# Kernel tuning notes

Measured on AMD Instinct MI355X. Metric: run time of the kernel, lower is better.

## Reference

```python
import jax, jax.numpy as jnp
import numpy as np

N = 20000   # nodes
E = 320000  # edges (before self-loops)
D = 128     # hidden_dim (= per-head out channels, concat=False)
H = 4       # heads
NEG_SLOPE = 0.2   # GATv2 leaky_relu default
LN_EPS = 1e-5


def setup_inputs() -> dict:
    key = jax.random.key(0)
    ks = jax.random.split(key, 12)
    s = 0.05
    w = lambda k, shp: (jax.random.normal(k, shp, jnp.float32) * s)
    return {
        "x": jax.random.normal(ks[0], (N, D), jnp.float32),
        "src": jax.random.randint(ks[1], (E,), 0, N, jnp.int32),
        "dst": jax.random.randint(ks[2], (E,), 0, N, jnp.int32),
        "Wl1": w(ks[3], (D, H * D)), "Wr1": w(ks[4], (D, H * D)),
        "att1": w(ks[5], (H, D)), "b1": jnp.zeros((D,), jnp.float32),
        "g1": jnp.ones((D,), jnp.float32), "be1": jnp.zeros((D,), jnp.float32),
        "Wl2": w(ks[6], (D, H * D)), "Wr2": w(ks[7], (D, H * D)),
        "att2": w(ks[8], (H, D)), "b2": jnp.zeros((D,), jnp.float32),
        "g2": jnp.ones((D,), jnp.float32), "be2": jnp.zeros((D,), jnp.float32),
    }


def gatv2_conv(x, src, dst, Wl, Wr, att, bias):
    """GATv2Conv with concat=False (mean over heads), share_weights=False."""
    n = x.shape[0]
    xl = (x @ Wl).reshape(n, H, D)  # source-side projection
    xr = (x @ Wr).reshape(n, H, D)  # target-side projection
    m = jax.nn.leaky_relu(xl[src] + xr[dst], NEG_SLOPE)     # [E', H, D]
    e = jnp.einsum('ehd,hd->eh', m, att)                     # [E', H]
    # segment softmax over edges grouped by destination node
    e_max = jax.ops.segment_max(e, dst, num_segments=n)      # [N, H]
    ex = jnp.exp(e - e_max[dst])
    denom = jax.ops.segment_sum(ex, dst, num_segments=n)     # [N, H]
    alpha = ex / (denom[dst] + 1e-16)                        # [E', H]
    out = jax.ops.segment_sum(alpha[:, :, None] * xl[src], dst, num_segments=n)
    return out.mean(axis=1) + bias                           # [N, D]


def layer_norm(x, g, b):
    mu = x.mean(axis=-1, keepdims=True)
    var = ((x - mu) ** 2).mean(axis=-1, keepdims=True)
    return (x - mu) * jax.lax.rsqrt(var + LN_EPS) * g + b


def reference(x, src, dst, Wl1, Wr1, att1, b1, g1, be1,
              Wl2, Wr2, att2, b2, g2, be2):
    n = x.shape[0]
    # PyG GATv2Conv default add_self_loops=True
    loops = jnp.arange(n, dtype=src.dtype)
    s = jnp.concatenate([src, loops])
    d = jnp.concatenate([dst, loops])

    h = gatv2_conv(x, s, d, Wl1, Wr1, att1, b1)
    h = layer_norm(h, g1, be1)
    h = jax.nn.relu(h + x)

    h2 = gatv2_conv(h, s, d, Wl2, Wr2, att2, b2)
    h2 = layer_norm(h2, g2, be2)
    return h2 + h
```

## Files before the change

kernel.cpp:

```cpp
#include <hip/hip_runtime.h>
#include <hip/hip_bf16.h>
#include <hip/hip_fp16.h>

#define NNODES 20000
#define MPAD   20480
#define NEDGES 320000
#define DIM    128
#define NH     4
#define ETOT   (NEDGES + NNODES)
#define LN_EPS 1e-5f

typedef unsigned char  u8;
typedef unsigned short u16;
typedef unsigned int   u32;

typedef _Float16 f16x2 __attribute__((ext_vector_type(2)));
typedef _Float16 f16x8 __attribute__((ext_vector_type(8)));
typedef float    f32x2 __attribute__((ext_vector_type(2)));
typedef float    f32x4 __attribute__((ext_vector_type(4)));

__device__ inline u16 f2h(float f) {
    _Float16 h = (_Float16)f;
    union { _Float16 h; u16 u; } v; v.h = h; return v.u;
}
__device__ inline f16x2 u2h2(u32 u) { union { u32 u; f16x2 h; } v; v.u = u; return v.h; }
__device__ inline u32 h22u(f16x2 h) { union { f16x2 h; u32 u; } v; v.h = h; return v.u; }
__device__ inline f16x2 habs2(f16x2 h) { return u2h2(h22u(h) & 0x7FFF7FFFu); }

#define GLDS16(g, l) __builtin_amdgcn_global_load_lds(                         \
    (const __attribute__((address_space(1))) void*)(g),                        \
    (__attribute__((address_space(3))) void*)(l), 16, 0, 0)


__global__ __launch_bounds__(256) void k_prep(const float* __restrict__ x, u16* __restrict__ xb,
                       const float* __restrict__ Wl1, const float* __restrict__ Wr1,
                       u16* __restrict__ Bt1,
                       const float* __restrict__ Wl2, const float* __restrict__ Wr2,
                       u16* __restrict__ Bt2,
                       int* __restrict__ deg) {
    const int b = blockIdx.x, t = threadIdx.x;
    const int gid = b * 256 + t;
    if (gid < NNODES) deg[gid] = 1;

    for (int j = gid; j < NNODES * 32; j += 256 * 256) {
        float4 v = ((const float4*)x)[j];
        ushort4 o;
        o.x = f2h(v.x); o.y = f2h(v.y); o.z = f2h(v.z); o.w = f2h(v.w);
        ((ushort4*)xb)[j] = o;
    }

    {
        const int m    = b >> 6;
        const int tile = b & 63;
        const int kt   = tile >> 4;
        const int nt   = tile & 15;
        const float* W = (m == 0) ? Wl1 : (m == 1) ? Wr1 : (m == 2) ? Wl2 : Wr2;
        u16* Bt        = (m < 2) ? Bt1 : Bt2;
        const int nbase = (m & 1) * 512 + nt * 32;

        __shared__ float lds[32][33];
        const int tx = t & 31, ty = t >> 5;
#pragma unroll
        for (int i = 0; i < 4; ++i) {
            int k = kt * 32 + ty + i * 8;
            lds[ty + i * 8][tx] = W[k * 512 + nt * 32 + tx];
        }
        __syncthreads();
#pragma unroll
        for (int i = 0; i < 4; ++i) {
            int nrow = nbase + ty + i * 8;
            Bt[nrow * 128 + kt * 32 + tx] = f2h(lds[tx][ty + i * 8]);
        }
    }
}


__global__ void k_hist(const int* __restrict__ dst, int* __restrict__ deg) {
    int i = blockIdx.x * blockDim.x + threadIdx.x;
    if (i < NEDGES) atomicAdd(&deg[dst[i]], 1);
}

__global__ __launch_bounds__(1024) void k_scan(const int* __restrict__ deg,
                                               int* __restrict__ row,
                                               int* __restrict__ cur) {
    __shared__ int part[1024];
    const int CH = 20;
    int t = threadIdx.x;
    int base = t * CH;
    int s = 0;
    int d[20];
    if (base < NNODES) {
#pragma unroll
        for (int q = 0; q < 5; ++q) {
            int4 v = ((const int4*)(deg + base))[q];
            d[q*4+0] = v.x; d[q*4+1] = v.y; d[q*4+2] = v.z; d[q*4+3] = v.w;
            s += v.x + v.y + v.z + v.w;
        }
    }
    part[t] = s;
    __syncthreads();
    for (int off = 1; off < 1024; off <<= 1) {
        int v = (t >= off) ? part[t - off] : 0;
        __syncthreads();
        part[t] += v;
        __syncthreads();
    }
    if (base < NNODES) {
        int run = (t == 0) ? 0 : part[t - 1];
#pragma unroll
        for (int i = 0; i < CH; i++) {
            row[base + i] = run; cur[base + i] = run; run += d[i];
        }
    }
    if (t == 1023) row[NNODES] = part[1023];
}

__global__ void k_scatter(const int* __restrict__ src, const int* __restrict__ dst,
                          int* __restrict__ col, int* __restrict__ cur) {
    int i = blockIdx.x * blockDim.x + threadIdx.x;
    if (i < NEDGES) {
        int d = dst[i];
        int pos = atomicAdd(&cur[d], 1);
        col[pos] = src[i];
    } else if (i < ETOT) {
        int n = i - NEDGES;
        int pos = atomicAdd(&cur[n], 1);
        col[pos] = n;
    }
}


__global__ __launch_bounds__(256, 2) void k_gemm_f16(const u16* __restrict__ A,
                                                     const u16* __restrict__ Bt,
                                                     u16* __restrict__ XL,
                                                     u16* __restrict__ XR) {
    __shared__ u16 smA[128 * 128];
    __shared__ u16 smB[128 * 128];
    const int L   = blockIdx.x;
    const int xcd = L & 7;
    const int w9  = L >> 3;
    const int bm  = (xcd * 20 + (w9 >> 3)) * 128;
    const int bn  = (w9 & 7) * 128;
    const int t  = threadIdx.x;
    const int w  = t >> 6;
    const int l  = t & 63;

    {
        char* smAb = (char*)smA;
        char* smBb = (char*)smB;
#pragma unroll
        for (int p = 0; p < 8; ++p) {
            int rbase = w * 32 + p * 4;
            int row   = rbase + (l >> 4);
            int j     = (l & 15) ^ (row & 7);
            const u16* ga = A  + (size_t)(bm + row) * 128 + j * 8;
            const u16* gb = Bt + (size_t)(bn + row) * 128 + j * 8;
            GLDS16(ga, smAb + rbase * 256);
            GLDS16(gb, smBb + rbase * 256);
        }
    }
    __syncthreads();

    const int wr  = (w >> 1) * 64;
    const int wc  = (w & 1) * 64;
    const int lr  = l & 15;
    const int lkb = (l >> 4) * 16;

    f32x4 acc[4][4] = {};

#pragma unroll
    for (int ks = 0; ks < 4; ++ks) {
        f16x8 af[4], bfr[4];
#pragma unroll
        for (int i = 0; i < 4; ++i) {
            int ra = wr + i * 16 + lr;
            af[i]  = *(const f16x8*)((const char*)smA +
                        ((ra * 256 + ks * 64 + lkb) ^ ((ra & 7) << 4)));
            int rb = wc + i * 16 + lr;
            bfr[i] = *(const f16x8*)((const char*)smB +
                        ((rb * 256 + ks * 64 + lkb) ^ ((rb & 7) << 4)));
        }
#pragma unroll
        for (int mi = 0; mi < 4; ++mi)
#pragma unroll
            for (int ni = 0; ni < 4; ++ni)
                acc[mi][ni] = __builtin_amdgcn_mfma_f32_16x16x32_f16(
                    bfr[ni], af[mi], acc[mi][ni], 0, 0, 0);
    }

    __syncthreads();
    u16* smC = smA;
    {
        const int n4 = (l >> 4) * 4;
#pragma unroll
        for (int mi = 0; mi < 4; ++mi) {
            int m = wr + mi * 16 + lr;
#pragma unroll
            for (int ni = 0; ni < 4; ++ni) {
                int n = wc + ni * 16 + n4;
                f32x4 v = acc[mi][ni];
                ushort4 o;
                o.x = f2h(v[0]); o.y = f2h(v[1]); o.z = f2h(v[2]); o.w = f2h(v[3]);
                *(ushort4*)((char*)smC + (m * 256 + ((n * 2) ^ ((m & 7) << 4)))) = o;
            }
        }
    }
    __syncthreads();
    {
        int r  = t >> 4;
        int cb = (t & 15) * 16;
        const bool left = (bn < 512);
        u16* base = left ? (XL + bn) : (XR + (bn - 512));
#pragma unroll
        for (int p = 0; p < 8; ++p) {
            int row = p * 16 + r;
            uint4 v = *(const uint4*)((const char*)smC +
                        (row * 256 + (cb ^ ((row & 7) << 4))));
            *(uint4*)(base + (size_t)(bm + row) * 512 + (cb >> 1)) = v;
        }
    }
}


__global__ __launch_bounds__(256) void k_attn(const u16* __restrict__ XL,
                                              const u16* __restrict__ XR,
                                              const float* __restrict__ att,
                                              const float* __restrict__ bias,
                                              const float* __restrict__ gamma,
                                              const float* __restrict__ beta,
                                              const int* __restrict__ row,
                                              const int* __restrict__ col,
                                              const float* __restrict__ res,
                                              float* __restrict__ out,
                                              u16* __restrict__ out_h,
                                              int relu_flag, int n0) {
    const int wid = __builtin_amdgcn_readfirstlane(threadIdx.x >> 6);
    const int n   = n0 + blockIdx.x * 4 + wid;
    const int l   = threadIdx.x & 63;
    const int h   = l >> 4;
    const int e   = l & 15;

    const f16x2 C06 = {(_Float16)0.6f, (_Float16)0.6f};
    const f16x2 C04 = {(_Float16)0.4f, (_Float16)0.4f};

    const size_t lane_off = h * 128 + e * 8;

    uint4 xru = *(const uint4*)(XR + (size_t)n * 512 + lane_off);
    f16x2 xr0 = u2h2(xru.x), xr1 = u2h2(xru.y), xr2 = u2h2(xru.z), xr3 = u2h2(xru.w);

    const float* ap = att + lane_off;
    float4 af0 = *(const float4*)(ap);
    float4 af1 = *(const float4*)(ap + 4);
    f16x2 at0 = {(_Float16)af0.x, (_Float16)af0.y};
    f16x2 at1 = {(_Float16)af0.z, (_Float16)af0.w};
    f16x2 at2 = {(_Float16)af1.x, (_Float16)af1.y};
    f16x2 at3 = {(_Float16)af1.z, (_Float16)af1.w};

    f16x2 acch[4] = {};
    float ssum = 0.f;

    const int beg = row[n], end = row[n + 1];

    int i = beg;
    int j = i + 2;
    {
        int c0 = col[i];
        int c1 = (i + 1 < end) ? col[i + 1] : c0;
        uint4 a0 = *(const uint4*)(XL + (size_t)c0 * 512 + lane_off);
        uint4 a1 = *(const uint4*)(XL + (size_t)c1 * 512 + lane_off);
        bool morej = j < end;
        int d0 = 0, d1 = 0;
        if (morej) { d0 = col[j]; d1 = (j + 1 < end) ? col[j + 1] : d0; }

        while (true) {
            uint4 b0, b1;
            if (morej) {
                b0 = *(const uint4*)(XL + (size_t)d0 * 512 + lane_off);
                b1 = *(const uint4*)(XL + (size_t)d1 * 512 + lane_off);
            }
            int k2 = j + 2;
            bool morek = morej && (k2 < end);
            int e0c = 0, e1c = 0;
            if (morek) { e0c = col[k2]; e1c = (k2 + 1 < end) ? col[k2 + 1] : e0c; }

            bool has2 = (i + 1 < end);
            float e0, e1;
            {
                f16x2 v0 = u2h2(a0.x) + xr0, v1 = u2h2(a0.y) + xr1;
                f16x2 v2 = u2h2(a0.z) + xr2, v3 = u2h2(a0.w) + xr3;
                f16x2 k0 = v0 * C06 + habs2(v0) * C04;
                f16x2 k1 = v1 * C06 + habs2(v1) * C04;
                f16x2 k2h = v2 * C06 + habs2(v2) * C04;
                f16x2 k3 = v3 * C06 + habs2(v3) * C04;
                e0 = __builtin_amdgcn_fdot2(k0, at0, 0.f, false);
                e0 = __builtin_amdgcn_fdot2(k1, at1, e0, false);
                e0 = __builtin_amdgcn_fdot2(k2h, at2, e0, false);
                e0 = __builtin_amdgcn_fdot2(k3, at3, e0, false);
            }
            {
                f16x2 v0 = u2h2(a1.x) + xr0, v1 = u2h2(a1.y) + xr1;
                f16x2 v2 = u2h2(a1.z) + xr2, v3 = u2h2(a1.w) + xr3;
                f16x2 k0 = v0 * C06 + habs2(v0) * C04;
                f16x2 k1 = v1 * C06 + habs2(v1) * C04;
                f16x2 k2h = v2 * C06 + habs2(v2) * C04;
                f16x2 k3 = v3 * C06 + habs2(v3) * C04;
                e1 = __builtin_amdgcn_fdot2(k0, at0, 0.f, false);
                e1 = __builtin_amdgcn_fdot2(k1, at1, e1, false);
                e1 = __builtin_amdgcn_fdot2(k2h, at2, e1, false);
                e1 = __builtin_amdgcn_fdot2(k3, at3, e1, false);
            }
#pragma unroll
            for (int m = 1; m < 16; m <<= 1) {
                e0 += __shfl_xor(e0, m, 64);
                e1 += __shfl_xor(e1, m, 64);
            }
            float p0 = __expf(e0);
            float p1 = has2 ? __expf(e1) : 0.f;
            ssum += p0 + p1;
            _Float16 ph0s = (_Float16)p0, ph1s = (_Float16)p1;
            f16x2 ph0 = {ph0s, ph0s};
            f16x2 ph1 = {ph1s, ph1s};
            acch[0] = acch[0] + ph0 * u2h2(a0.x) + ph1 * u2h2(a1.x);
            acch[1] = acch[1] + ph0 * u2h2(a0.y) + ph1 * u2h2(a1.y);
            acch[2] = acch[2] + ph0 * u2h2(a0.z) + ph1 * u2h2(a1.z);
            acch[3] = acch[3] + ph0 * u2h2(a0.w) + ph1 * u2h2(a1.w);

            if (!morej) break;
            a0 = b0; a1 = b1;
            i = j; j = k2;
            d0 = e0c; d1 = e1c;
            morej = morek;
        }
    }

    float acc[8];
    {
        f32x2 c;
        c = __builtin_convertvector(acch[0], f32x2); acc[0] = c[0]; acc[1] = c[1];
        c = __builtin_convertvector(acch[1], f32x2); acc[2] = c[0]; acc[3] = c[1];
        c = __builtin_convertvector(acch[2], f32x2); acc[4] = c[0]; acc[5] = c[1];
        c = __builtin_convertvector(acch[3], f32x2); acc[6] = c[0]; acc[7] = c[1];
    }
    float inv = 1.f / (ssum + 1e-16f);
#pragma unroll
    for (int jj = 0; jj < 8; ++jj) acc[jj] *= inv;
#pragma unroll
    for (int jj = 0; jj < 8; ++jj) acc[jj] += __shfl_xor(acc[jj], 16, 64);
#pragma unroll
    for (int jj = 0; jj < 8; ++jj) acc[jj] += __shfl_xor(acc[jj], 32, 64);

    if (h == 0) {
        const int dd = e * 8;
        float4 b40 = *(const float4*)(bias + dd);
        float4 b41 = *(const float4*)(bias + dd + 4);
        float y[8];
        y[0] = acc[0]*0.25f + b40.x; y[1] = acc[1]*0.25f + b40.y;
        y[2] = acc[2]*0.25f + b40.z; y[3] = acc[3]*0.25f + b40.w;
        y[4] = acc[4]*0.25f + b41.x; y[5] = acc[5]*0.25f + b41.y;
        y[6] = acc[6]*0.25f + b41.z; y[7] = acc[7]*0.25f + b41.w;

        float s1 = 0.f, s2 = 0.f;
#pragma unroll
        for (int jj = 0; jj < 8; ++jj) { s1 += y[jj]; s2 += y[jj]*y[jj]; }
#pragma unroll
        for (int m = 1; m < 16; m <<= 1) {
            s1 += __shfl_xor(s1, m, 64);
            s2 += __shfl_xor(s2, m, 64);
        }
        float mu = s1 * (1.f / 128.f);
        float var = s2 * (1.f / 128.f) - mu * mu;
        float rstd = rsqrtf(var + LN_EPS);

        float4 g40 = *(const float4*)(gamma + dd);
        float4 g41 = *(const float4*)(gamma + dd + 4);
        float4 e40 = *(const float4*)(beta + dd);
        float4 e41 = *(const float4*)(beta + dd + 4);
        float4 r40 = *(const float4*)(res + (size_t)n * 128 + dd);
        float4 r41 = *(const float4*)(res + (size_t)n * 128 + dd + 4);
        float g[8] = {g40.x,g40.y,g40.z,g40.w,g41.x,g41.y,g41.z,g41.w};
        float be[8] = {e40.x,e40.y,e40.z,e40.w,e41.x,e41.y,e41.z,e41.w};
        float r[8] = {r40.x,r40.y,r40.z,r40.w,r41.x,r41.y,r41.z,r41.w};
#pragma unroll
        for (int jj = 0; jj < 8; ++jj) {
            y[jj] = (y[jj] - mu) * rstd * g[jj] + be[jj] + r[jj];
            if (relu_flag) y[jj] = fmaxf(y[jj], 0.f);
        }
        float4 o0 = {y[0],y[1],y[2],y[3]};
        float4 o1 = {y[4],y[5],y[6],y[7]};
        *(float4*)(out + (size_t)n * 128 + dd)     = o0;
        *(float4*)(out + (size_t)n * 128 + dd + 4) = o1;
        if (out_h) {
            ushort4 oh0, oh1;
            oh0.x = f2h(y[0]); oh0.y = f2h(y[1]); oh0.z = f2h(y[2]); oh0.w = f2h(y[3]);
            oh1.x = f2h(y[4]); oh1.y = f2h(y[5]); oh1.z = f2h(y[6]); oh1.w = f2h(y[7]);
            *(ushort4*)(out_h + (size_t)n * 128 + dd)     = oh0;
            *(ushort4*)(out_h + (size_t)n * 128 + dd + 4) = oh1;
        }
    }
}


extern "C" void kernel_launch(void* const* d_in, const int* in_sizes, int n_in,
                              void* d_out, int out_size, void* d_ws, size_t ws_size,
                              hipStream_t stream) {
    const float* x    = (const float*)d_in[0];
    const int*   src  = (const int*)d_in[1];
    const int*   dst  = (const int*)d_in[2];
    const float* Wl1  = (const float*)d_in[3];
    const float* Wr1  = (const float*)d_in[4];
    const float* att1 = (const float*)d_in[5];
    const float* b1   = (const float*)d_in[6];
    const float* g1   = (const float*)d_in[7];
    const float* be1  = (const float*)d_in[8];
    const float* Wl2  = (const float*)d_in[9];
    const float* Wr2  = (const float*)d_in[10];
    const float* att2 = (const float*)d_in[11];
    const float* b2   = (const float*)d_in[12];
    const float* g2   = (const float*)d_in[13];
    const float* be2  = (const float*)d_in[14];
    float* out = (float*)d_out;

    char* ws = (char*)d_ws;
    size_t off = 0;
    u16*   xlb  = (u16*)(ws + off);   off += (size_t)MPAD * 512 * 2;
    u16*   xrb  = (u16*)(ws + off);   off += (size_t)MPAD * 512 * 2;
    u16*   xb   = (u16*)(ws + off);   off += (size_t)MPAD * 128 * 2;
    float* hbuf = (float*)(ws + off); off += (size_t)NNODES * 128 * 4;
    u16*   Bt1  = (u16*)(ws + off);   off += (size_t)1024 * 128 * 2;
    u16*   Bt2  = (u16*)(ws + off);   off += (size_t)1024 * 128 * 2;
    int*   deg  = (int*)(ws + off);   off += (size_t)NNODES * 4;
    int*   rowp = (int*)(ws + off);   off += (size_t)(NNODES + 1) * 4;
    int*   cur  = (int*)(ws + off);   off += (size_t)NNODES * 4;
    int*   col  = (int*)(ws + off);   off += (size_t)ETOT * 4;

    k_prep<<<256, 256, 0, stream>>>(x, xb, Wl1, Wr1, Bt1, Wl2, Wr2, Bt2, deg);
    k_hist<<<(NEDGES + 255) / 256, 256, 0, stream>>>(dst, deg);
    k_scan<<<1, 1024, 0, stream>>>(deg, rowp, cur);
    k_scatter<<<(ETOT + 255) / 256, 256, 0, stream>>>(src, dst, col, cur);

    const int HALF = NNODES / 2;

    k_gemm_f16<<<MPAD / 128 * 8, 256, 0, stream>>>(xb, Bt1, xlb, xrb);
    k_attn<<<HALF / 4, 256, 0, stream>>>(xlb, xrb, att1, b1, g1, be1, rowp, col,
                                         x, hbuf, xb, 1, 0);
    k_attn<<<HALF / 4, 256, 0, stream>>>(xlb, xrb, att1, b1, g1, be1, rowp, col,
                                         x, hbuf, xb, 1, HALF);
    k_gemm_f16<<<MPAD / 128 * 8, 256, 0, stream>>>(xb, Bt2, xlb, xrb);
    k_attn<<<HALF / 4, 256, 0, stream>>>(xlb, xrb, att2, b2, g2, be2, rowp, col,
                                         hbuf, out, (u16*)nullptr, 0, 0);
    k_attn<<<HALF / 4, 256, 0, stream>>>(xlb, xrb, att2, b2, g2, be2, rowp, col,
                                         hbuf, out, (u16*)nullptr, 0, HALF);
}
```

Measured before the change: 202.8 us.

## Quantize source projections to int8 with per-head scales for edge gather

Adds a k_quant pass that converts the fp16 XL projection into int8 with one fp16 scale per node and head. The attention kernel then gathers 8-byte int8 rows instead of 16-byte fp16 rows and dequantizes in registers, which halves gather traffic on this bandwidth-bound edge loop. The software-pipelined prefetch loop is replaced by a simpler two-edge loop, and the two half-graph attention launches are merged into one. The cost is an extra kernel pass per layer, added dequantization arithmetic, and int8 quantization error in both the attention scores and the aggregated features.

```diff
diff --git a/kernel.cpp b/kernel.cpp
--- a/kernel.cpp
+++ b/kernel.cpp
@@ -14,14 +14,18 @@
 typedef unsigned short u16;
 typedef unsigned int   u32;
 
-typedef _Float16 f16x2 __attribute__((ext_vector_type(2)));
-typedef _Float16 f16x8 __attribute__((ext_vector_type(8)));
-typedef float    f32x2 __attribute__((ext_vector_type(2)));
-typedef float    f32x4 __attribute__((ext_vector_type(4)));
+typedef _Float16    f16x2 __attribute__((ext_vector_type(2)));
+typedef _Float16    f16x8 __attribute__((ext_vector_type(8)));
+typedef float       f32x2 __attribute__((ext_vector_type(2)));
+typedef float       f32x4 __attribute__((ext_vector_type(4)));
+typedef signed char i8x8  __attribute__((ext_vector_type(8)));
 
 __device__ inline u16 f2h(float f) {
     _Float16 h = (_Float16)f;
     union { _Float16 h; u16 u; } v; v.h = h; return v.u;
+}
+__device__ inline _Float16 bits2h(u16 b) {
+    union { u16 u; _Float16 h; } v; v.u = b; return v.h;
 }
 __device__ inline f16x2 u2h2(u32 u) { union { u32 u; f16x2 h; } v; v.u = u; return v.h; }
 __device__ inline u32 h22u(f16x2 h) { union { f16x2 h; u32 u; } v; v.h = h; return v.u; }
@@ -222,7 +226,49 @@
 }
 
 
-__global__ __launch_bounds__(256) void k_attn(const u16* __restrict__ XL,
+__global__ __launch_bounds__(256) void k_quant(const u16* __restrict__ XL,
+                                               u8* __restrict__ XLq,
+                                               u16* __restrict__ scales) {
+    const int wid = threadIdx.x >> 6;
+    const int n   = blockIdx.x * 4 + wid;
+    const int l   = threadIdx.x & 63;
+    const int h   = l >> 4, e = l & 15;
+
+    uint4 v = *(const uint4*)(XL + (size_t)n * 512 + h * 128 + e * 8);
+    float vf[8];
+    {
+        f32x2 c;
+        c = __builtin_convertvector(u2h2(v.x), f32x2); vf[0] = c[0]; vf[1] = c[1];
+        c = __builtin_convertvector(u2h2(v.y), f32x2); vf[2] = c[0]; vf[3] = c[1];
+        c = __builtin_convertvector(u2h2(v.z), f32x2); vf[4] = c[0]; vf[5] = c[1];
+        c = __builtin_convertvector(u2h2(v.w), f32x2); vf[6] = c[0]; vf[7] = c[1];
+    }
+    float m = 0.f;
+#pragma unroll
+    for (int k = 0; k < 8; ++k) m = fmaxf(m, fabsf(vf[k]));
+#pragma unroll
+    for (int off = 1; off < 16; off <<= 1) m = fmaxf(m, __shfl_xor(m, off, 64));
+
+    float scale = m * (1.f / 127.f);
+    float inv   = (m > 0.f) ? (127.f / m) : 0.f;
+
+    int q[8];
+#pragma unroll
+    for (int k = 0; k < 8; ++k) {
+        int qi = (int)__builtin_rintf(vf[k] * inv);
+        qi = qi > 127 ? 127 : (qi < -127 ? -127 : qi);
+        q[k] = qi;
+    }
+    u32 lo = (q[0] & 255) | ((q[1] & 255) << 8) | ((q[2] & 255) << 16) | ((q[3] & 255) << 24);
+    u32 hi = (q[4] & 255) | ((q[5] & 255) << 8) | ((q[6] & 255) << 16) | ((q[7] & 255) << 24);
+    uint2 o; o.x = lo; o.y = hi;
+    *(uint2*)(XLq + (size_t)n * 512 + h * 128 + e * 8) = o;
+    if (e == 0) scales[n * 4 + h] = f2h(scale);
+}
+
+
+__global__ __launch_bounds__(256) void k_attn(const u8*  __restrict__ XLq,
+                                              const u16* __restrict__ scales,
                                               const u16* __restrict__ XR,
                                               const float* __restrict__ att,
                                               const float* __restrict__ bias,
@@ -233,9 +279,9 @@
                                               const float* __restrict__ res,
                                               float* __restrict__ out,
                                               u16* __restrict__ out_h,
-                                              int relu_flag, int n0) {
+                                              int relu_flag) {
     const int wid = __builtin_amdgcn_readfirstlane(threadIdx.x >> 6);
-    const int n   = n0 + blockIdx.x * 4 + wid;
+    const int n   = blockIdx.x * 4 + wid;
     const int l   = threadIdx.x & 63;
     const int h   = l >> 4;
     const int e   = l & 15;
@@ -243,7 +289,7 @@
     const f16x2 C06 = {(_Float16)0.6f, (_Float16)0.6f};
     const f16x2 C04 = {(_Float16)0.4f, (_Float16)0.4f};
 
-    const size_t lane_off = h * 128 + e * 8;
+    const int lane_off = h * 128 + e * 8;
 
     uint4 xru = *(const uint4*)(XR + (size_t)n * 512 + lane_off);
     f16x2 xr0 = u2h2(xru.x), xr1 = u2h2(xru.y), xr2 = u2h2(xru.z), xr3 = u2h2(xru.w);
@@ -261,76 +307,77 @@
 
     const int beg = row[n], end = row[n + 1];
 
-    int i = beg;
-    int j = i + 2;
-    {
-        int c0 = col[i];
-        int c1 = (i + 1 < end) ? col[i + 1] : c0;
-        uint4 a0 = *(const uint4*)(XL + (size_t)c0 * 512 + lane_off);
-        uint4 a1 = *(const uint4*)(XL + (size_t)c1 * 512 + lane_off);
-        bool morej = j < end;
-        int d0 = 0, d1 = 0;
-        if (morej) { d0 = col[j]; d1 = (j + 1 < end) ? col[j + 1] : d0; }
-
-        while (true) {
-            uint4 b0, b1;
-            if (morej) {
-                b0 = *(const uint4*)(XL + (size_t)d0 * 512 + lane_off);
-                b1 = *(const uint4*)(XL + (size_t)d1 * 512 + lane_off);
-            }
-            int k2 = j + 2;
-            bool morek = morej && (k2 < end);
-            int e0c = 0, e1c = 0;
-            if (morek) { e0c = col[k2]; e1c = (k2 + 1 < end) ? col[k2 + 1] : e0c; }
-
-            bool has2 = (i + 1 < end);
-            float e0, e1;
-            {
-                f16x2 v0 = u2h2(a0.x) + xr0, v1 = u2h2(a0.y) + xr1;
-                f16x2 v2 = u2h2(a0.z) + xr2, v3 = u2h2(a0.w) + xr3;
-                f16x2 k0 = v0 * C06 + habs2(v0) * C04;
-                f16x2 k1 = v1 * C06 + habs2(v1) * C04;
-                f16x2 k2h = v2 * C06 + habs2(v2) * C04;
-                f16x2 k3 = v3 * C06 + habs2(v3) * C04;
-                e0 = __builtin_amdgcn_fdot2(k0, at0, 0.f, false);
-                e0 = __builtin_amdgcn_fdot2(k1, at1, e0, false);
-                e0 = __builtin_amdgcn_fdot2(k2h, at2, e0, false);
-                e0 = __builtin_amdgcn_fdot2(k3, at3, e0, false);
-            }
-            {
-                f16x2 v0 = u2h2(a1.x) + xr0, v1 = u2h2(a1.y) + xr1;
-                f16x2 v2 = u2h2(a1.z) + xr2, v3 = u2h2(a1.w) + xr3;
-                f16x2 k0 = v0 * C06 + habs2(v0) * C04;
-                f16x2 k1 = v1 * C06 + habs2(v1) * C04;
-                f16x2 k2h = v2 * C06 + habs2(v2) * C04;
-                f16x2 k3 = v3 * C06 + habs2(v3) * C04;
-                e1 = __builtin_amdgcn_fdot2(k0, at0, 0.f, false);
-                e1 = __builtin_amdgcn_fdot2(k1, at1, e1, false);
-                e1 = __builtin_amdgcn_fdot2(k2h, at2, e1, false);
-                e1 = __builtin_amdgcn_fdot2(k3, at3, e1, false);
-            }
-#pragma unroll
-            for (int m = 1; m < 16; m <<= 1) {
-                e0 += __shfl_xor(e0, m, 64);
-                e1 += __shfl_xor(e1, m, 64);
-            }
-            float p0 = __expf(e0);
-            float p1 = has2 ? __expf(e1) : 0.f;
-            ssum += p0 + p1;
-            _Float16 ph0s = (_Float16)p0, ph1s = (_Float16)p1;
-            f16x2 ph0 = {ph0s, ph0s};
-            f16x2 ph1 = {ph1s, ph1s};
-            acch[0] = acch[0] + ph0 * u2h2(a0.x) + ph1 * u2h2(a1.x);
-            acch[1] = acch[1] + ph0 * u2h2(a0.y) + ph1 * u2h2(a1.y);
-            acch[2] = acch[2] + ph0 * u2h2(a0.z) + ph1 * u2h2(a1.z);
-            acch[3] = acch[3] + ph0 * u2h2(a0.w) + ph1 * u2h2(a1.w);
-
-            if (!morej) break;
-            a0 = b0; a1 = b1;
-            i = j; j = k2;
-            d0 = e0c; d1 = e1c;
-            morej = morek;
-        }
+    for (int i = beg; i < end; i += 2) {
+        int s0 = col[i];
+        bool has2 = (i + 1 < end);
+        int s1 = has2 ? col[i + 1] : s0;
+
+        uint2 a0 = *(const uint2*)(XLq + (size_t)s0 * 512 + lane_off);
+        uint2 a1 = *(const uint2*)(XLq + (size_t)s1 * 512 + lane_off);
+        _Float16 sh0 = bits2h(scales[s0 * 4 + h]);
+        _Float16 sh1 = bits2h(scales[s1 * 4 + h]);
+        f16x2 s0h2 = {sh0, sh0};
+        f16x2 s1h2 = {sh1, sh1};
+
+        f16x8 q0, q1;
+        {
+            union { uint2 u; i8x8 c; } uc;
+            uc.u = a0; q0 = __builtin_convertvector(uc.c, f16x8);
+            uc.u = a1; q1 = __builtin_convertvector(uc.c, f16x8);
+        }
+        f16x2 q00 = __builtin_shufflevector(q0, q0, 0, 1);
+        f16x2 q01 = __builtin_shufflevector(q0, q0, 2, 3);
+        f16x2 q02 = __builtin_shufflevector(q0, q0, 4, 5);
+        f16x2 q03 = __builtin_shufflevector(q0, q0, 6, 7);
+        f16x2 q10 = __builtin_shufflevector(q1, q1, 0, 1);
+        f16x2 q11 = __builtin_shufflevector(q1, q1, 2, 3);
+        f16x2 q12 = __builtin_shufflevector(q1, q1, 4, 5);
+        f16x2 q13 = __builtin_shufflevector(q1, q1, 6, 7);
+
+        float e0, e1;
+        {
+            f16x2 v0 = q00 * s0h2 + xr0, v1 = q01 * s0h2 + xr1;
+            f16x2 v2 = q02 * s0h2 + xr2, v3 = q03 * s0h2 + xr3;
+            f16x2 k0 = v0 * C06 + habs2(v0) * C04;
+            f16x2 k1 = v1 * C06 + habs2(v1) * C04;
+            f16x2 k2 = v2 * C06 + habs2(v2) * C04;
+            f16x2 k3 = v3 * C06 + habs2(v3) * C04;
+            e0 = __builtin_amdgcn_fdot2(k0, at0, 0.f, false);
+            e0 = __builtin_amdgcn_fdot2(k1, at1, e0, false);
+            e0 = __builtin_amdgcn_fdot2(k2, at2, e0, false);
+            e0 = __builtin_amdgcn_fdot2(k3, at3, e0, false);
+        }
+        {
+            f16x2 v0 = q10 * s1h2 + xr0, v1 = q11 * s1h2 + xr1;
+            f16x2 v2 = q12 * s1h2 + xr2, v3 = q13 * s1h2 + xr3;
+            f16x2 k0 = v0 * C06 + habs2(v0) * C04;
+            f16x2 k1 = v1 * C06 + habs2(v1) * C04;
+            f16x2 k2 = v2 * C06 + habs2(v2) * C04;
+            f16x2 k3 = v3 * C06 + habs2(v3) * C04;
+            e1 = __builtin_amdgcn_fdot2(k0, at0, 0.f, false);
+            e1 = __builtin_amdgcn_fdot2(k1, at1, e1, false);
+            e1 = __builtin_amdgcn_fdot2(k2, at2, e1, false);
+            e1 = __builtin_amdgcn_fdot2(k3, at3, e1, false);
+        }
+
+#pragma unroll
+        for (int m = 1; m < 16; m <<= 1) {
+            e0 += __shfl_xor(e0, m, 64);
+            e1 += __shfl_xor(e1, m, 64);
+        }
+
+        float p0 = __expf(e0);
+        float p1 = has2 ? __expf(e1) : 0.f;
+        ssum += p0 + p1;
+
+        _Float16 ph0s = (_Float16)(p0 * (float)sh0);
+        _Float16 ph1s = (_Float16)(p1 * (float)sh1);
+        f16x2 ph0 = {ph0s, ph0s};
+        f16x2 ph1 = {ph1s, ph1s};
+        acch[0] = acch[0] + ph0 * q00 + ph1 * q10;
+        acch[1] = acch[1] + ph0 * q01 + ph1 * q11;
+        acch[2] = acch[2] + ph0 * q02 + ph1 * q12;
+        acch[3] = acch[3] + ph0 * q03 + ph1 * q13;
     }
 
     float acc[8];
@@ -424,6 +471,8 @@
     size_t off = 0;
     u16*   xlb  = (u16*)(ws + off);   off += (size_t)MPAD * 512 * 2;
     u16*   xrb  = (u16*)(ws + off);   off += (size_t)MPAD * 512 * 2;
+    u8*    xlq  = (u8*)(ws + off);    off += (size_t)NNODES * 512;
+    u16*   scl  = (u16*)(ws + off);   off += (size_t)NNODES * 4 * 2;
     u16*   xb   = (u16*)(ws + off);   off += (size_t)MPAD * 128 * 2;
     float* hbuf = (float*)(ws + off); off += (size_t)NNODES * 128 * 4;
     u16*   Bt1  = (u16*)(ws + off);   off += (size_t)1024 * 128 * 2;
@@ -438,16 +487,12 @@
     k_scan<<<1, 1024, 0, stream>>>(deg, rowp, cur);
     k_scatter<<<(ETOT + 255) / 256, 256, 0, stream>>>(src, dst, col, cur);
 
-    const int HALF = NNODES / 2;
-
     k_gemm_f16<<<MPAD / 128 * 8, 256, 0, stream>>>(xb, Bt1, xlb, xrb);
-    k_attn<<<HALF / 4, 256, 0, stream>>>(xlb, xrb, att1, b1, g1, be1, rowp, col,
-                                         x, hbuf, xb, 1, 0);
-    k_attn<<<HALF / 4, 256, 0, stream>>>(xlb, xrb, att1, b1, g1, be1, rowp, col,
-                                         x, hbuf, xb, 1, HALF);
+    k_quant<<<NNODES / 4, 256, 0, stream>>>(xlb, xlq, scl);
+    k_attn<<<NNODES / 4, 256, 0, stream>>>(xlq, scl, xrb, att1, b1, g1, be1, rowp, col,
+                                           x, hbuf, xb, 1);
     k_gemm_f16<<<MPAD / 128 * 8, 256, 0, stream>>>(xb, Bt2, xlb, xrb);
-    k_attn<<<HALF / 4, 256, 0, stream>>>(xlb, xrb, att2, b2, g2, be2, rowp, col,
-                                         hbuf, out, (u16*)nullptr, 0, 0);
-    k_attn<<<HALF / 4, 256, 0, stream>>>(xlb, xrb, att2, b2, g2, be2, rowp, col,
-                                         hbuf, out, (u16*)nullptr, 0, HALF);
-}
+    k_quant<<<NNODES / 4, 256, 0, stream>>>(xlb, xlq, scl);
+    k_attn<<<NNODES / 4, 256, 0, stream>>>(xlq, scl, xrb, att2, b2, g2, be2, rowp, col,
+                                           hbuf, out, (u16*)nullptr, 0);
+}
```

After: 190.8 us. -5.9%, faster.
